# Optimization experiments

Measured on AMD Instinct MI355X. Metric: run time of the kernel, lower is better.

Reference implementation:

```python
import jax, jax.numpy as jnp
import numpy as np

B, T, DL, DM, H = 8, 4096, 1024, 1024, 8
HD = min(DL, DM) // H  # 128


def setup_inputs() -> dict:
    key = jax.random.key(0)
    ks = jax.random.split(key, 8)
    s = 0.02

    def w(k, shape):
        return jax.random.normal(k, shape, jnp.float32) * s

    return {
        "liquid_repr": jax.random.normal(ks[0], (B, T, DL), jnp.float32),
        "mamba_repr": jax.random.normal(ks[1], (B, T, DM), jnp.float32),
        "Wlq": w(ks[2], (DL, H * HD)), "blq": jnp.zeros((H * HD,), jnp.float32),
        "Wmkv": w(ks[3], (DM, 2 * H * HD)), "bmkv": jnp.zeros((2 * H * HD,), jnp.float32),
        "Wmq": w(ks[4], (DM, H * HD)), "bmq": jnp.zeros((H * HD,), jnp.float32),
        "Wlkv": w(ks[5], (DL, 2 * H * HD)), "blkv": jnp.zeros((2 * H * HD,), jnp.float32),
        "Wlo": w(ks[6], (H * HD, DL)), "blo": jnp.zeros((DL,), jnp.float32),
        "Wmo": w(ks[7], (H * HD, DM)), "bmo": jnp.zeros((DM,), jnp.float32),
    }


def _attn(q, k, v):
    # q,k,v: [B,T,H,HD]. Faithful to torch: matmul over last two dims ->
    # scores [B,T,H,H] (attention over the heads axis per timestep).
    scores = jnp.einsum('bthd,btgd->bthg', q, k) / jnp.sqrt(jnp.float32(HD))
    w = jax.nn.softmax(scores, axis=-1)
    return jnp.einsum('bthg,btgd->bthd', w, v)


def reference(liquid_repr, mamba_repr, Wlq, blq, Wmkv, bmkv, Wmq, bmq,
              Wlkv, blkv, Wlo, blo, Wmo, bmo):
    b, t, _ = liquid_repr.shape
    # liquid queries mamba
    q_l = (liquid_repr @ Wlq + blq).reshape(b, t, H, HD)
    kv_m = (mamba_repr @ Wmkv + bmkv).reshape(b, t, H, 2 * HD)
    k_m, v_m = kv_m[..., :HD], kv_m[..., HD:]
    a_l = _attn(q_l, k_m, v_m).reshape(b, t, H * HD)
    enhanced_liquid = liquid_repr + a_l @ Wlo + blo
    # mamba queries liquid
    q_m = (mamba_repr @ Wmq + bmq).reshape(b, t, H, HD)
    kv_l = (liquid_repr @ Wlkv + blkv).reshape(b, t, H, 2 * HD)
    k_l, v_l = kv_l[..., :HD], kv_l[..., HD:]
    a_m = _attn(q_m, k_l, v_l).reshape(b, t, H * HD)
    enhanced_mamba = mamba_repr + a_m @ Wmo + bmo
    return enhanced_liquid, enhanced_mamba
```

## Files before the change

kernel.cpp:

```cpp
#include <hip/hip_runtime.h>

typedef unsigned short u16;
typedef unsigned int u32;

typedef __attribute__((ext_vector_type(4))) float floatx4;
typedef __attribute__((ext_vector_type(8))) __bf16 bf16x8;

typedef __attribute__((address_space(3))) u32 lds_u32_t;
typedef __attribute__((address_space(1))) u32 glb_u32_t;

__device__ __forceinline__ void gld_lds16(const u16* g, u16* l) {
    __builtin_amdgcn_global_load_lds((glb_u32_t*)g, (lds_u32_t*)l, 16, 0, 0);
}

__device__ __forceinline__ u16 f2bf(float f) {
    u32 u = __float_as_uint(f);
    u += 0x7fffu + ((u >> 16) & 1u);
    return (u16)(u >> 16);
}
__device__ __forceinline__ u32 pk2(float a, float b) {
    u32 x = __float_as_uint(a), y = __float_as_uint(b);
    x += 0x7fffu + ((x >> 16) & 1u);
    y += 0x7fffu + ((y >> 16) & 1u);
    return (x >> 16) | (y & 0xffff0000u);
}

#define BM 128
#define BN 128
#define BK 32

__global__ __launch_bounds__(256) void convert_f32_bf16(
    const float* __restrict__ src, u16* __restrict__ dst)
{
    const size_t i = ((size_t)blockIdx.x * 256 + threadIdx.x) * 8;
    float4 a = *(const float4*)(src + i);
    float4 b = *(const float4*)(src + i + 4);
    *(uint4*)(dst + i) = make_uint4(pk2(a.x, a.y), pk2(a.z, a.w),
                                    pk2(b.x, b.y), pk2(b.z, b.w));
}

__global__ __launch_bounds__(256, 2) void gemm_a16_c16(
    const u16* __restrict__ A, int lda,
    const u16* __restrict__ Bt,
    const float* __restrict__ bias,
    u16* __restrict__ C, int ldc,
    int K)
{
    __shared__ __align__(16) u16 sA[BM * BK];
    __shared__ __align__(16) u16 sB[BN * BK];
    const int tid  = threadIdx.x;
    const int bm   = blockIdx.x, bn = blockIdx.y;
    const int lane = tid & 63,  wave = tid >> 6;
    const int wm   = wave >> 1, wn   = wave & 1;
    const int l15  = lane & 15, quad = lane >> 4;

    const int sr = tid >> 2;
    const int sc = (tid & 3) * 8;
    const u16* gA0 = A  + (size_t)(bm * BM + sr) * lda + sc;
    const u16* gA1 = gA0 + (size_t)64 * lda;
    const u16* gB0 = Bt + (size_t)(bn * BN + sr) * K + sc;
    const u16* gB1 = gB0 + (size_t)64 * K;
    u16* lA0 = &sA[tid * 8];  u16* lA1 = &sA[2048 + tid * 8];
    u16* lB0 = &sB[tid * 8];  u16* lB1 = &sB[2048 + tid * 8];

    floatx4 acc[4][4] = {};

    for (int k0 = 0; k0 < K; k0 += BK) {
        __syncthreads();
        gld_lds16(gA0 + k0, lA0);
        gld_lds16(gA1 + k0, lA1);
        gld_lds16(gB0 + k0, lB0);
        gld_lds16(gB1 + k0, lB1);
        __syncthreads();

        bf16x8 af[4], bfr[4];
#pragma unroll
        for (int mi = 0; mi < 4; mi++)
            af[mi] = *(const bf16x8*)&sA[(wm * 64 + mi * 16 + l15) * BK + quad * 8];
#pragma unroll
        for (int ni = 0; ni < 4; ni++)
            bfr[ni] = *(const bf16x8*)&sB[(wn * 64 + ni * 16 + l15) * BK + quad * 8];
#pragma unroll
        for (int mi = 0; mi < 4; mi++)
#pragma unroll
            for (int ni = 0; ni < 4; ni++)
                acc[mi][ni] = __builtin_amdgcn_mfma_f32_16x16x32_bf16(
                    af[mi], bfr[ni], acc[mi][ni], 0, 0, 0);
    }

    const int row0 = bm * BM + wm * 64 + quad * 4;
    const int col0 = bn * BN + wn * 64 + l15;
#pragma unroll
    for (int mi = 0; mi < 4; mi++) {
#pragma unroll
        for (int ni = 0; ni < 4; ni++) {
            const int col = col0 + ni * 16;
            const float bv = bias[col];
#pragma unroll
            for (int r = 0; r < 4; r++) {
                const int row = row0 + mi * 16 + r;
                C[(size_t)row * ldc + col] = f2bf(acc[mi][ni][r] + bv);
            }
        }
    }
}

__global__ __launch_bounds__(256, 2) void gemm_a16_c32(
    const u16* __restrict__ A, int lda,
    const u16* __restrict__ Bt,
    const float* __restrict__ bias,
    const float* __restrict__ R, int ldr,
    float* __restrict__ C, int ldc,
    int K)
{
    __shared__ __align__(16) u16 sA[BM * BK];
    __shared__ __align__(16) u16 sB[BN * BK];
    const int tid  = threadIdx.x;
    const int bm   = blockIdx.x, bn = blockIdx.y;
    const int lane = tid & 63,  wave = tid >> 6;
    const int wm   = wave >> 1, wn   = wave & 1;
    const int l15  = lane & 15, quad = lane >> 4;

    const int sr = tid >> 2;
    const int sc = (tid & 3) * 8;
    const u16* gA0 = A  + (size_t)(bm * BM + sr) * lda + sc;
    const u16* gA1 = gA0 + (size_t)64 * lda;
    const u16* gB0 = Bt + (size_t)(bn * BN + sr) * K + sc;
    const u16* gB1 = gB0 + (size_t)64 * K;
    u16* lA0 = &sA[tid * 8];  u16* lA1 = &sA[2048 + tid * 8];
    u16* lB0 = &sB[tid * 8];  u16* lB1 = &sB[2048 + tid * 8];

    floatx4 acc[4][4] = {};

    for (int k0 = 0; k0 < K; k0 += BK) {
        __syncthreads();
        gld_lds16(gA0 + k0, lA0);
        gld_lds16(gA1 + k0, lA1);
        gld_lds16(gB0 + k0, lB0);
        gld_lds16(gB1 + k0, lB1);
        __syncthreads();

        bf16x8 af[4], bfr[4];
#pragma unroll
        for (int mi = 0; mi < 4; mi++)
            af[mi] = *(const bf16x8*)&sA[(wm * 64 + mi * 16 + l15) * BK + quad * 8];
#pragma unroll
        for (int ni = 0; ni < 4; ni++)
            bfr[ni] = *(const bf16x8*)&sB[(wn * 64 + ni * 16 + l15) * BK + quad * 8];
#pragma unroll
        for (int mi = 0; mi < 4; mi++)
#pragma unroll
            for (int ni = 0; ni < 4; ni++)
                acc[mi][ni] = __builtin_amdgcn_mfma_f32_16x16x32_bf16(
                    af[mi], bfr[ni], acc[mi][ni], 0, 0, 0);
    }

    const int row0 = bm * BM + wm * 64 + quad * 4;
    const int col0 = bn * BN + wn * 64 + l15;
#pragma unroll
    for (int mi = 0; mi < 4; mi++) {
#pragma unroll
        for (int ni = 0; ni < 4; ni++) {
            const int col = col0 + ni * 16;
            const float bv = bias[col];
#pragma unroll
            for (int r = 0; r < 4; r++) {
                const int row = row0 + mi * 16 + r;
                C[(size_t)row * ldc + col] =
                    acc[mi][ni][r] + bv + R[(size_t)row * ldr + col];
            }
        }
    }
}

#define AW 136

__global__ __launch_bounds__(256) void attn8(
    const u16* Q,
    const u16* __restrict__ KV,
    u16* O,
    int qstride, int kvstride)
{
    __shared__ __align__(16) float lds[4 * (3 * 8 * AW + 64)];
    const int wid = threadIdx.x >> 6, lane = threadIdx.x & 63;
    float* qs = lds + wid * (3 * 8 * AW + 64);
    float* ks = qs + 8 * AW;
    float* vs = ks + 8 * AW;
    float* ws = vs + 8 * AW;
    const size_t pos = (size_t)blockIdx.x * 4 + wid;
    const u16* qrow  = Q  + pos * qstride;
    const u16* kvrow = KV + pos * kvstride;

#pragma unroll
    for (int it = 0; it < 2; it++) {
        int vi = lane + 64 * it;
        int h = vi >> 4, c = (vi & 15) * 8;
        uint4 r = *(const uint4*)(qrow + vi * 8);
        float f0 = __uint_as_float(r.x << 16), f1 = __uint_as_float(r.x & 0xffff0000u);
        float f2 = __uint_as_float(r.y << 16), f3 = __uint_as_float(r.y & 0xffff0000u);
        float f4 = __uint_as_float(r.z << 16), f5 = __uint_as_float(r.z & 0xffff0000u);
        float f6 = __uint_as_float(r.w << 16), f7 = __uint_as_float(r.w & 0xffff0000u);
        float4* d = (float4*)&qs[h * AW + c];
        d[0] = make_float4(f0, f1, f2, f3);
        d[1] = make_float4(f4, f5, f6, f7);
    }
#pragma unroll
    for (int it = 0; it < 4; it++) {
        int vi = lane + 64 * it;
        int g = vi >> 5, c = (vi & 31) * 8;
        uint4 r = *(const uint4*)(kvrow + vi * 8);
        float f0 = __uint_as_float(r.x << 16), f1 = __uint_as_float(r.x & 0xffff0000u);
        float f2 = __uint_as_float(r.y << 16), f3 = __uint_as_float(r.y & 0xffff0000u);
        float f4 = __uint_as_float(r.z << 16), f5 = __uint_as_float(r.z & 0xffff0000u);
        float f6 = __uint_as_float(r.w << 16), f7 = __uint_as_float(r.w & 0xffff0000u);
        float* base = (c < 128) ? &ks[g * AW + c] : &vs[g * AW + (c - 128)];
        ((float4*)base)[0] = make_float4(f0, f1, f2, f3);
        ((float4*)base)[1] = make_float4(f4, f5, f6, f7);
    }
    __syncthreads();

    const int h = lane >> 3, g = lane & 7;
    float s = 0.f;
#pragma unroll 8
    for (int d = 0; d < 128; d += 4) {
        float4 qv = *(const float4*)&qs[h * AW + d];
        float4 kv = *(const float4*)&ks[g * AW + d];
        s += qv.x * kv.x + qv.y * kv.y + qv.z * kv.z + qv.w * kv.w;
    }
    s *= 0.08838834764831845f;
    float m = s;
    m = fmaxf(m, __shfl_xor(m, 1, 64));
    m = fmaxf(m, __shfl_xor(m, 2, 64));
    m = fmaxf(m, __shfl_xor(m, 4, 64));
    float p = __expf(s - m);
    float sum = p;
    sum += __shfl_xor(sum, 1, 64);
    sum += __shfl_xor(sum, 2, 64);
    sum += __shfl_xor(sum, 4, 64);
    ws[lane] = p / sum;
    __syncthreads();

    const int db = lane & 7;
    float o[16];
#pragma unroll
    for (int j = 0; j < 16; j++) o[j] = 0.f;
#pragma unroll
    for (int g2 = 0; g2 < 8; g2++) {
        float wv = ws[h * 8 + g2];
        const float* vr = &vs[g2 * AW + db * 16];
#pragma unroll
        for (int j = 0; j < 16; j++) o[j] += wv * vr[j];
    }
    u16* orow = O + pos * qstride + h * 128 + db * 16;
    u32 pk[8];
#pragma unroll
    for (int j = 0; j < 8; j++)
        pk[j] = (u32)f2bf(o[2 * j]) | ((u32)f2bf(o[2 * j + 1]) << 16);
    ((uint4*)orow)[0] = make_uint4(pk[0], pk[1], pk[2], pk[3]);
    ((uint4*)orow)[1] = make_uint4(pk[4], pk[5], pk[6], pk[7]);
}

__global__ __launch_bounds__(256) void transpose_f32_bf16(
    const float* __restrict__ src, u16* __restrict__ dst, int K, int N)
{
    __shared__ float tile[32][33];
    const int tx = threadIdx.x & 31, ty = threadIdx.x >> 5;
    const int c0 = blockIdx.x * 32, r0 = blockIdx.y * 32;
#pragma unroll
    for (int i = 0; i < 4; i++)
        tile[ty + i * 8][tx] = src[(size_t)(r0 + ty + i * 8) * N + c0 + tx];
    __syncthreads();
#pragma unroll
    for (int i = 0; i < 4; i++)
        dst[(size_t)(c0 + ty + i * 8) * K + r0 + tx] = f2bf(tile[tx][ty + i * 8]);
}

extern "C" void kernel_launch(void* const* d_in, const int* in_sizes, int n_in,
                              void* d_out, int out_size, void* d_ws, size_t ws_size,
                              hipStream_t stream) {
    const float* liquid = (const float*)d_in[0];
    const float* mamba  = (const float*)d_in[1];
    const float* Wlq  = (const float*)d_in[2];
    const float* blq  = (const float*)d_in[3];
    const float* Wmkv = (const float*)d_in[4];
    const float* bmkv = (const float*)d_in[5];
    const float* Wmq  = (const float*)d_in[6];
    const float* bmq  = (const float*)d_in[7];
    const float* Wlkv = (const float*)d_in[8];
    const float* blkv = (const float*)d_in[9];
    const float* Wlo  = (const float*)d_in[10];
    const float* blo  = (const float*)d_in[11];
    const float* Wmo  = (const float*)d_in[12];
    const float* bmo  = (const float*)d_in[13];
    float* out = (float*)d_out;

    u16* p = (u16*)d_ws;
    u16* WtLq  = p; p += (size_t)1024 * 1024;
    u16* WtLkv = p; p += (size_t)2048 * 1024;
    u16* WtMq  = p; p += (size_t)1024 * 1024;
    u16* WtMkv = p; p += (size_t)2048 * 1024;
    u16* WtLo  = p; p += (size_t)1024 * 1024;
    u16* WtMo  = p; p += (size_t)1024 * 1024;
    u16* Q  = p; p += (size_t)32768 * 1024;
    u16* KV = p;

    u16* Lb = (u16*)(out + (size_t)32768 * 1024);
    u16* Mb = Lb + (size_t)32768 * 1024;

    transpose_f32_bf16<<<dim3(32, 32), 256, 0, stream>>>(Wlq,  WtLq,  1024, 1024);
    transpose_f32_bf16<<<dim3(64, 32), 256, 0, stream>>>(Wlkv, WtLkv, 1024, 2048);
    transpose_f32_bf16<<<dim3(32, 32), 256, 0, stream>>>(Wmq,  WtMq,  1024, 1024);
    transpose_f32_bf16<<<dim3(64, 32), 256, 0, stream>>>(Wmkv, WtMkv, 1024, 2048);
    transpose_f32_bf16<<<dim3(32, 32), 256, 0, stream>>>(Wlo,  WtLo,  1024, 1024);
    transpose_f32_bf16<<<dim3(32, 32), 256, 0, stream>>>(Wmo,  WtMo,  1024, 1024);

    convert_f32_bf16<<<16384, 256, 0, stream>>>(liquid, Lb);
    convert_f32_bf16<<<16384, 256, 0, stream>>>(mamba,  Mb);

    gemm_a16_c16<<<dim3(256, 8),  256, 0, stream>>>(Lb, 1024, WtLq,  blq,  Q,  1024, 1024);
    gemm_a16_c16<<<dim3(256, 16), 256, 0, stream>>>(Mb, 1024, WtMkv, bmkv, KV, 2048, 1024);
    attn8<<<8192, 256, 0, stream>>>(Q, KV, Q, 1024, 2048);
    gemm_a16_c32<<<dim3(256, 8),  256, 0, stream>>>(Q, 1024, WtLo, blo, liquid, 1024,
                                                    out, 1024, 1024);

    gemm_a16_c16<<<dim3(256, 8),  256, 0, stream>>>(Mb, 1024, WtMq,  bmq,  Q,  1024, 1024);
    gemm_a16_c16<<<dim3(256, 16), 256, 0, stream>>>(Lb, 1024, WtLkv, blkv, KV, 2048, 1024);
    attn8<<<8192, 256, 0, stream>>>(Q, KV, Q, 1024, 2048);
    gemm_a16_c32<<<dim3(256, 8),  256, 0, stream>>>(Q, 1024, WtMo, bmo, mamba, 1024,
                                                    out + (size_t)32768 * 1024, 1024, 1024);
}
```

Before: 1.354 ms.

## Replace GEMMs with 256x256-tile 8-wave double-buffered pipelined kernel

Swaps the simple 128x128, BK=32 single-buffer GEMMs for one templated kernel. It uses 256x256 tiles, 512 threads, K-steps of 64 with double-buffered LDS, an XOR swizzle against bank conflicts, and interleaves global-to-LDS staging with MFMA quarters under s_setprio. It also remaps block indices so neighbouring blocks share A/B tiles in cache. The aim is to hide load latency and raise MFMA utilization in the projection GEMMs, which dominate runtime. The cost is heavy LDS use (128KB per block), high register pressure, and hand-placed waitcnt/barrier logic that is fragile.

```diff
diff --git a/kernel.cpp b/kernel.cpp
--- a/kernel.cpp
+++ b/kernel.cpp
@@ -25,9 +25,143 @@
     return (x >> 16) | (y & 0xffff0000u);
 }
 
-#define BM 128
-#define BN 128
-#define BK 32
+#define BARRIER() asm volatile("s_barrier" ::: "memory")
+#define WAITVM(N) asm volatile("s_waitcnt vmcnt(" #N ")" ::: "memory")
+#define SWZ(d) ((d) ^ ((((d) >> 9) & 1) << 5))
+#define MFMA16(a, b, c) __builtin_amdgcn_mfma_f32_16x16x32_bf16(a, b, c, 0, 0, 0)
+
+__device__ __forceinline__ void stage_half(const u16* __restrict__ g, int ld,
+                                           u16* halfdst, int wid, int lane)
+{
+#pragma unroll
+    for (int j = 0; j < 2; ++j) {
+        const int clin = wid * 128 + j * 64 + lane;
+        const int csrc = clin ^ (((clin >> 5) & 1) << 1);
+        gld_lds16(g + (size_t)(csrc >> 3) * ld + (csrc & 7) * 8,
+                  halfdst + clin * 8);
+    }
+}
+
+template<int EPI>
+__global__ __launch_bounds__(512, 2) void gemm8p(
+    const u16* __restrict__ A, int lda,
+    const u16* __restrict__ Bt,
+    const float* __restrict__ bias,
+    const float* __restrict__ R, int ldr,
+    u16* __restrict__ Cb, float* __restrict__ Cf, int ldc,
+    int K, int nbn)
+{
+    __shared__ __align__(16) u16 lds[65536];
+    const int tid = threadIdx.x, lane = tid & 63, wid = tid >> 6;
+    const int wm = wid >> 2, wn = wid & 3;
+    const int l15 = lane & 15, quad = lane >> 4;
+    const char* ldsb = (const char*)lds;
+    const int wmB = wm * 16384;
+    const int wnB = (wn >> 1) * 16384;
+    const int wnR = (wn & 1) * 64;
+    const int qb = quad * 16;
+
+    const int nwg = (int)gridDim.x;
+    const int sw = ((int)blockIdx.x & 7) * (nwg >> 3) + ((int)blockIdx.x >> 3);
+    const int bn = sw % nbn, bm = sw / nbn;
+    const int rowA0 = bm * 256, rowB0 = bn * 256;
+
+#define STG_A(t, h) stage_half(A + (size_t)(rowA0 + (h) * 128) * lda + (t) * 64, lda, \
+                               lds + ((t) & 1) * 32768 + (h) * 8192, wid, lane)
+#define STG_B(t, h) stage_half(Bt + (size_t)(rowB0 + (h) * 128) * K + (t) * 64, K, \
+                               lds + ((t) & 1) * 32768 + 16384 + (h) * 8192, wid, lane)
+#define LDA8(P, MQ, mi, ks) \
+    (*(const bf16x8*)(ldsb + (P) * 65536 + wmB + \
+        SWZ(((MQ) * 64 + (mi) * 16 + l15) * 128 + (ks) * 64 + qb)))
+#define LDB8(P, nf, ks) \
+    (*(const bf16x8*)(ldsb + (P) * 65536 + 32768 + wnB + \
+        SWZ((wnR + (nf) * 16 + l15) * 128 + (ks) * 64 + qb)))
+#define READ_A(P, MQ) \
+    _Pragma("unroll") \
+    for (int mi = 0; mi < 4; ++mi) { aF[mi*2] = LDA8(P, MQ, mi, 0); aF[mi*2+1] = LDA8(P, MQ, mi, 1); }
+#define READ_B(P, NQ) \
+    _Pragma("unroll") \
+    for (int ni = 0; ni < 2; ++ni) { bF[NQ][ni*2] = LDB8(P, (NQ)*2+ni, 0); bF[NQ][ni*2+1] = LDB8(P, (NQ)*2+ni, 1); }
+#define MFMA_Q(MQ, NQ) \
+    __builtin_amdgcn_s_setprio(1); \
+    _Pragma("unroll") \
+    for (int mi = 0; mi < 4; ++mi) \
+        _Pragma("unroll") \
+        for (int ni = 0; ni < 2; ++ni) { \
+            acc[(MQ)*4+mi][(NQ)*2+ni] = MFMA16(aF[mi*2],   bF[NQ][ni*2],   acc[(MQ)*4+mi][(NQ)*2+ni]); \
+            acc[(MQ)*4+mi][(NQ)*2+ni] = MFMA16(aF[mi*2+1], bF[NQ][ni*2+1], acc[(MQ)*4+mi][(NQ)*2+ni]); \
+        } \
+    __builtin_amdgcn_s_setprio(0);
+
+    floatx4 acc[8][4] = {};
+    bf16x8 aF[8], bF[2][4];
+
+    const int NI = K >> 7;
+
+    STG_B(0, 0); STG_B(0, 1); STG_A(0, 0); STG_A(0, 1);
+    STG_B(1, 0); STG_B(1, 1);
+    WAITVM(4);
+    BARRIER();
+
+    for (int i = 0; i < NI; ++i) {
+        const int tE = 2 * i, tO = 2 * i + 1;
+        const bool pre = (i + 1 < NI);
+
+        READ_A(0, 0); READ_B(0, 0);
+        STG_A(tO, 0);
+        BARRIER(); MFMA_Q(0, 0); BARRIER();
+
+        READ_B(0, 1);
+        STG_A(tO, 1);
+        BARRIER(); MFMA_Q(0, 1); BARRIER();
+
+        READ_A(0, 1);
+        if (pre) STG_B(tE + 2, 0);
+        BARRIER(); MFMA_Q(1, 1); BARRIER();
+
+        if (pre) { STG_B(tE + 2, 1); WAITVM(4); } else { WAITVM(0); }
+        BARRIER(); MFMA_Q(1, 0); BARRIER();
+
+        READ_A(1, 0); READ_B(1, 0);
+        if (pre) STG_A(tE + 2, 0);
+        BARRIER(); MFMA_Q(0, 0); BARRIER();
+
+        READ_B(1, 1);
+        if (pre) STG_A(tE + 2, 1);
+        BARRIER(); MFMA_Q(0, 1); BARRIER();
+
+        READ_A(1, 1);
+        if (pre) STG_B(tO + 2, 0);
+        BARRIER(); MFMA_Q(1, 1); BARRIER();
+
+        if (pre) STG_B(tO + 2, 1);
+        WAITVM(4);
+        BARRIER(); MFMA_Q(1, 0); BARRIER();
+    }
+
+#pragma unroll
+    for (int mq = 0; mq < 2; ++mq)
+#pragma unroll
+        for (int mi = 0; mi < 4; ++mi) {
+            const int row = rowA0 + wm * 128 + mq * 64 + mi * 16 + quad * 4;
+#pragma unroll
+            for (int nf = 0; nf < 4; ++nf) {
+                const int col = rowB0 + wn * 64 + nf * 16 + l15;
+                const float bv = bias[col];
+                const floatx4 v = acc[mq * 4 + mi][nf];
+                if (EPI == 0) {
+#pragma unroll
+                    for (int r = 0; r < 4; ++r)
+                        Cb[(size_t)(row + r) * ldc + col] = f2bf(v[r] + bv);
+                } else {
+#pragma unroll
+                    for (int r = 0; r < 4; ++r)
+                        Cf[(size_t)(row + r) * ldc + col] =
+                            v[r] + bv + R[(size_t)(row + r) * ldr + col];
+                }
+            }
+        }
+}
 
 __global__ __launch_bounds__(256) void convert_f32_bf16(
     const float* __restrict__ src, u16* __restrict__ dst)
@@ -37,140 +171,6 @@
     float4 b = *(const float4*)(src + i + 4);
     *(uint4*)(dst + i) = make_uint4(pk2(a.x, a.y), pk2(a.z, a.w),
                                     pk2(b.x, b.y), pk2(b.z, b.w));
-}
-
-__global__ __launch_bounds__(256, 2) void gemm_a16_c16(
-    const u16* __restrict__ A, int lda,
-    const u16* __restrict__ Bt,
-    const float* __restrict__ bias,
-    u16* __restrict__ C, int ldc,
-    int K)
-{
-    __shared__ __align__(16) u16 sA[BM * BK];
-    __shared__ __align__(16) u16 sB[BN * BK];
-    const int tid  = threadIdx.x;
-    const int bm   = blockIdx.x, bn = blockIdx.y;
-    const int lane = tid & 63,  wave = tid >> 6;
-    const int wm   = wave >> 1, wn   = wave & 1;
-    const int l15  = lane & 15, quad = lane >> 4;
-
-    const int sr = tid >> 2;
-    const int sc = (tid & 3) * 8;
-    const u16* gA0 = A  + (size_t)(bm * BM + sr) * lda + sc;
-    const u16* gA1 = gA0 + (size_t)64 * lda;
-    const u16* gB0 = Bt + (size_t)(bn * BN + sr) * K + sc;
-    const u16* gB1 = gB0 + (size_t)64 * K;
-    u16* lA0 = &sA[tid * 8];  u16* lA1 = &sA[2048 + tid * 8];
-    u16* lB0 = &sB[tid * 8];  u16* lB1 = &sB[2048 + tid * 8];
-
-    floatx4 acc[4][4] = {};
-
-    for (int k0 = 0; k0 < K; k0 += BK) {
-        __syncthreads();
-        gld_lds16(gA0 + k0, lA0);
-        gld_lds16(gA1 + k0, lA1);
-        gld_lds16(gB0 + k0, lB0);
-        gld_lds16(gB1 + k0, lB1);
-        __syncthreads();
-
-        bf16x8 af[4], bfr[4];
-#pragma unroll
-        for (int mi = 0; mi < 4; mi++)
-            af[mi] = *(const bf16x8*)&sA[(wm * 64 + mi * 16 + l15) * BK + quad * 8];
-#pragma unroll
-        for (int ni = 0; ni < 4; ni++)
-            bfr[ni] = *(const bf16x8*)&sB[(wn * 64 + ni * 16 + l15) * BK + quad * 8];
-#pragma unroll
-        for (int mi = 0; mi < 4; mi++)
-#pragma unroll
-            for (int ni = 0; ni < 4; ni++)
-                acc[mi][ni] = __builtin_amdgcn_mfma_f32_16x16x32_bf16(
-                    af[mi], bfr[ni], acc[mi][ni], 0, 0, 0);
-    }
-
-    const int row0 = bm * BM + wm * 64 + quad * 4;
-    const int col0 = bn * BN + wn * 64 + l15;
-#pragma unroll
-    for (int mi = 0; mi < 4; mi++) {
-#pragma unroll
-        for (int ni = 0; ni < 4; ni++) {
-            const int col = col0 + ni * 16;
-            const float bv = bias[col];
-#pragma unroll
-            for (int r = 0; r < 4; r++) {
-                const int row = row0 + mi * 16 + r;
-                C[(size_t)row * ldc + col] = f2bf(acc[mi][ni][r] + bv);
-            }
-        }
-    }
-}
-
-__global__ __launch_bounds__(256, 2) void gemm_a16_c32(
-    const u16* __restrict__ A, int lda,
-    const u16* __restrict__ Bt,
-    const float* __restrict__ bias,
-    const float* __restrict__ R, int ldr,
-    float* __restrict__ C, int ldc,
-    int K)
-{
-    __shared__ __align__(16) u16 sA[BM * BK];
-    __shared__ __align__(16) u16 sB[BN * BK];
-    const int tid  = threadIdx.x;
-    const int bm   = blockIdx.x, bn = blockIdx.y;
-    const int lane = tid & 63,  wave = tid >> 6;
-    const int wm   = wave >> 1, wn   = wave & 1;
-    const int l15  = lane & 15, quad = lane >> 4;
-
-    const int sr = tid >> 2;
-    const int sc = (tid & 3) * 8;
-    const u16* gA0 = A  + (size_t)(bm * BM + sr) * lda + sc;
-    const u16* gA1 = gA0 + (size_t)64 * lda;
-    const u16* gB0 = Bt + (size_t)(bn * BN + sr) * K + sc;
-    const u16* gB1 = gB0 + (size_t)64 * K;
-    u16* lA0 = &sA[tid * 8];  u16* lA1 = &sA[2048 + tid * 8];
-    u16* lB0 = &sB[tid * 8];  u16* lB1 = &sB[2048 + tid * 8];
-
-    floatx4 acc[4][4] = {};
-
-    for (int k0 = 0; k0 < K; k0 += BK) {
-        __syncthreads();
-        gld_lds16(gA0 + k0, lA0);
-        gld_lds16(gA1 + k0, lA1);
-        gld_lds16(gB0 + k0, lB0);
-        gld_lds16(gB1 + k0, lB1);
-        __syncthreads();
-
-        bf16x8 af[4], bfr[4];
-#pragma unroll
-        for (int mi = 0; mi < 4; mi++)
-            af[mi] = *(const bf16x8*)&sA[(wm * 64 + mi * 16 + l15) * BK + quad * 8];
-#pragma unroll
-        for (int ni = 0; ni < 4; ni++)
-            bfr[ni] = *(const bf16x8*)&sB[(wn * 64 + ni * 16 + l15) * BK + quad * 8];
-#pragma unroll
-        for (int mi = 0; mi < 4; mi++)
-#pragma unroll
-            for (int ni = 0; ni < 4; ni++)
-                acc[mi][ni] = __builtin_amdgcn_mfma_f32_16x16x32_bf16(
-                    af[mi], bfr[ni], acc[mi][ni], 0, 0, 0);
-    }
-
-    const int row0 = bm * BM + wm * 64 + quad * 4;
-    const int col0 = bn * BN + wn * 64 + l15;
-#pragma unroll
-    for (int mi = 0; mi < 4; mi++) {
-#pragma unroll
-        for (int ni = 0; ni < 4; ni++) {
-            const int col = col0 + ni * 16;
-            const float bv = bias[col];
-#pragma unroll
-            for (int r = 0; r < 4; r++) {
-                const int row = row0 + mi * 16 + r;
-                C[(size_t)row * ldc + col] =
-                    acc[mi][ni][r] + bv + R[(size_t)row * ldr + col];
-            }
-        }
-    }
 }
 
 #define AW 136
@@ -317,15 +317,19 @@
     convert_f32_bf16<<<16384, 256, 0, stream>>>(liquid, Lb);
     convert_f32_bf16<<<16384, 256, 0, stream>>>(mamba,  Mb);
 
-    gemm_a16_c16<<<dim3(256, 8),  256, 0, stream>>>(Lb, 1024, WtLq,  blq,  Q,  1024, 1024);
-    gemm_a16_c16<<<dim3(256, 16), 256, 0, stream>>>(Mb, 1024, WtMkv, bmkv, KV, 2048, 1024);
+    gemm8p<0><<<512,  512, 0, stream>>>(Lb, 1024, WtLq,  blq,  nullptr, 0,
+                                        Q,  nullptr, 1024, 1024, 4);
+    gemm8p<0><<<1024, 512, 0, stream>>>(Mb, 1024, WtMkv, bmkv, nullptr, 0,
+                                        KV, nullptr, 2048, 1024, 8);
     attn8<<<8192, 256, 0, stream>>>(Q, KV, Q, 1024, 2048);
-    gemm_a16_c32<<<dim3(256, 8),  256, 0, stream>>>(Q, 1024, WtLo, blo, liquid, 1024,
-                                                    out, 1024, 1024);
-
-    gemm_a16_c16<<<dim3(256, 8),  256, 0, stream>>>(Mb, 1024, WtMq,  bmq,  Q,  1024, 1024);
-    gemm_a16_c16<<<dim3(256, 16), 256, 0, stream>>>(Lb, 1024, WtLkv, blkv, KV, 2048, 1024);
+    gemm8p<1><<<512,  512, 0, stream>>>(Q, 1024, WtLo, blo, liquid, 1024,
+                                        nullptr, out, 1024, 1024, 4);
+
+    gemm8p<0><<<512,  512, 0, stream>>>(Mb, 1024, WtMq,  bmq,  nullptr, 0,
+                                        Q,  nullptr, 1024, 1024, 4);
+    gemm8p<0><<<1024, 512, 0, stream>>>(Lb, 1024, WtLkv, blkv, nullptr, 0,
+                                        KV, nullptr, 2048, 1024, 8);
     attn8<<<8192, 256, 0, stream>>>(Q, KV, Q, 1024, 2048);
-    gemm_a16_c32<<<dim3(256, 8),  256, 0, stream>>>(Q, 1024, WtMo, bmo, mamba, 1024,
-                                                    out + (size_t)32768 * 1024, 1024, 1024);
-}
+    gemm8p<1><<<512,  512, 0, stream>>>(Q, 1024, WtMo, bmo, mamba, 1024,
+                                        nullptr, out + (size_t)32768 * 1024, 1024, 1024, 4);
+}
```

Result: slower. 2.121 ms (+56.7%).

## Double GEMM K-tile to 64 and XOR-swizzle LDS layout to avoid bank conflicts

Applied to the files above, without the earlier changes.

Both bf16 GEMM kernels now stage a 64-wide K slice per iteration instead of 32. This halves the number of barrier pairs per output tile and gives each sync two MFMA sub-steps. The LDS layout is XOR-swizzled: global loads place 16-byte chunks at permuted positions and the fragment reads apply the matching swizzle, which is meant to remove LDS bank conflicts on the 128-byte rows. LDS use per block doubles to 32 KB, which could affect occupancy at two blocks per CU.

```diff
diff --git a/kernel.cpp b/kernel.cpp
--- a/kernel.cpp
+++ b/kernel.cpp
@@ -25,9 +25,11 @@
     return (x >> 16) | (y & 0xffff0000u);
 }
 
+#define SWZ(d) ((d) ^ ((((d) >> 7) & 7) << 4))
+
 #define BM 128
 #define BN 128
-#define BK 32
+#define BK 64
 
 __global__ __launch_bounds__(256) void convert_f32_bf16(
     const float* __restrict__ src, u16* __restrict__ dst)
@@ -53,39 +55,41 @@
     const int lane = tid & 63,  wave = tid >> 6;
     const int wm   = wave >> 1, wn   = wave & 1;
     const int l15  = lane & 15, quad = lane >> 4;
-
-    const int sr = tid >> 2;
-    const int sc = (tid & 3) * 8;
-    const u16* gA0 = A  + (size_t)(bm * BM + sr) * lda + sc;
-    const u16* gA1 = gA0 + (size_t)64 * lda;
-    const u16* gB0 = Bt + (size_t)(bn * BN + sr) * K + sc;
-    const u16* gB1 = gB0 + (size_t)64 * K;
-    u16* lA0 = &sA[tid * 8];  u16* lA1 = &sA[2048 + tid * 8];
-    u16* lB0 = &sB[tid * 8];  u16* lB1 = &sB[2048 + tid * 8];
+    const char* sAb = (const char*)sA;
+    const char* sBb = (const char*)sB;
 
     floatx4 acc[4][4] = {};
 
     for (int k0 = 0; k0 < K; k0 += BK) {
         __syncthreads();
-        gld_lds16(gA0 + k0, lA0);
-        gld_lds16(gA1 + k0, lA1);
-        gld_lds16(gB0 + k0, lB0);
-        gld_lds16(gB1 + k0, lB1);
+#pragma unroll
+        for (int j = 0; j < 4; ++j) {
+            const int clin = tid + j * 256;
+            const int csrc = clin ^ ((clin >> 3) & 7);
+            const int r = csrc >> 3, c = (csrc & 7) * 8;
+            gld_lds16(A  + (size_t)(bm * BM + r) * lda + k0 + c, &sA[clin * 8]);
+            gld_lds16(Bt + (size_t)(bn * BN + r) * K   + k0 + c, &sB[clin * 8]);
+        }
         __syncthreads();
 
-        bf16x8 af[4], bfr[4];
-#pragma unroll
-        for (int mi = 0; mi < 4; mi++)
-            af[mi] = *(const bf16x8*)&sA[(wm * 64 + mi * 16 + l15) * BK + quad * 8];
-#pragma unroll
-        for (int ni = 0; ni < 4; ni++)
-            bfr[ni] = *(const bf16x8*)&sB[(wn * 64 + ni * 16 + l15) * BK + quad * 8];
-#pragma unroll
-        for (int mi = 0; mi < 4; mi++)
+#pragma unroll
+        for (int ks = 0; ks < 2; ++ks) {
+            bf16x8 af[4], bfr[4];
+#pragma unroll
+            for (int mi = 0; mi < 4; mi++)
+                af[mi] = *(const bf16x8*)(sAb +
+                    SWZ((wm * 64 + mi * 16 + l15) * 128 + ks * 64 + quad * 16));
 #pragma unroll
             for (int ni = 0; ni < 4; ni++)
-                acc[mi][ni] = __builtin_amdgcn_mfma_f32_16x16x32_bf16(
-                    af[mi], bfr[ni], acc[mi][ni], 0, 0, 0);
+                bfr[ni] = *(const bf16x8*)(sBb +
+                    SWZ((wn * 64 + ni * 16 + l15) * 128 + ks * 64 + quad * 16));
+#pragma unroll
+            for (int mi = 0; mi < 4; mi++)
+#pragma unroll
+                for (int ni = 0; ni < 4; ni++)
+                    acc[mi][ni] = __builtin_amdgcn_mfma_f32_16x16x32_bf16(
+                        af[mi], bfr[ni], acc[mi][ni], 0, 0, 0);
+        }
     }
 
     const int row0 = bm * BM + wm * 64 + quad * 4;
@@ -120,39 +124,41 @@
     const int lane = tid & 63,  wave = tid >> 6;
     const int wm   = wave >> 1, wn   = wave & 1;
     const int l15  = lane & 15, quad = lane >> 4;
-
-    const int sr = tid >> 2;
-    const int sc = (tid & 3) * 8;
-    const u16* gA0 = A  + (size_t)(bm * BM + sr) * lda + sc;
-    const u16* gA1 = gA0 + (size_t)64 * lda;
-    const u16* gB0 = Bt + (size_t)(bn * BN + sr) * K + sc;
-    const u16* gB1 = gB0 + (size_t)64 * K;
-    u16* lA0 = &sA[tid * 8];  u16* lA1 = &sA[2048 + tid * 8];
-    u16* lB0 = &sB[tid * 8];  u16* lB1 = &sB[2048 + tid * 8];
+    const char* sAb = (const char*)sA;
+    const char* sBb = (const char*)sB;
 
     floatx4 acc[4][4] = {};
 
     for (int k0 = 0; k0 < K; k0 += BK) {
         __syncthreads();
-        gld_lds16(gA0 + k0, lA0);
-        gld_lds16(gA1 + k0, lA1);
-        gld_lds16(gB0 + k0, lB0);
-        gld_lds16(gB1 + k0, lB1);
+#pragma unroll
+        for (int j = 0; j < 4; ++j) {
+            const int clin = tid + j * 256;
+            const int csrc = clin ^ ((clin >> 3) & 7);
+            const int r = csrc >> 3, c = (csrc & 7) * 8;
+            gld_lds16(A  + (size_t)(bm * BM + r) * lda + k0 + c, &sA[clin * 8]);
+            gld_lds16(Bt + (size_t)(bn * BN + r) * K   + k0 + c, &sB[clin * 8]);
+        }
         __syncthreads();
 
-        bf16x8 af[4], bfr[4];
-#pragma unroll
-        for (int mi = 0; mi < 4; mi++)
-            af[mi] = *(const bf16x8*)&sA[(wm * 64 + mi * 16 + l15) * BK + quad * 8];
-#pragma unroll
-        for (int ni = 0; ni < 4; ni++)
-            bfr[ni] = *(const bf16x8*)&sB[(wn * 64 + ni * 16 + l15) * BK + quad * 8];
-#pragma unroll
-        for (int mi = 0; mi < 4; mi++)
+#pragma unroll
+        for (int ks = 0; ks < 2; ++ks) {
+            bf16x8 af[4], bfr[4];
+#pragma unroll
+            for (int mi = 0; mi < 4; mi++)
+                af[mi] = *(const bf16x8*)(sAb +
+                    SWZ((wm * 64 + mi * 16 + l15) * 128 + ks * 64 + quad * 16));
 #pragma unroll
             for (int ni = 0; ni < 4; ni++)
-                acc[mi][ni] = __builtin_amdgcn_mfma_f32_16x16x32_bf16(
-                    af[mi], bfr[ni], acc[mi][ni], 0, 0, 0);
+                bfr[ni] = *(const bf16x8*)(sBb +
+                    SWZ((wn * 64 + ni * 16 + l15) * 128 + ks * 64 + quad * 16));
+#pragma unroll
+            for (int mi = 0; mi < 4; mi++)
+#pragma unroll
+                for (int ni = 0; ni < 4; ni++)
+                    acc[mi][ni] = __builtin_amdgcn_mfma_f32_16x16x32_bf16(
+                        af[mi], bfr[ni], acc[mi][ni], 0, 0, 0);
+        }
     }
 
     const int row0 = bm * BM + wm * 64 + quad * 4;
```

After: 1.357 ms. Within noise of the previous version (+0.2%).
